# Kernel optimization log

Hardware: AMD Instinct MI355X
Metric: run time of the kernel (lower is better)

## Reference

```python
import jax, jax.numpy as jnp
import numpy as np

# dims: P patches, D=N_azi*N_ele directions, R=P*D radiances, E COO edges,
# T echogram samples, F rfft bins
P, D, R, E, T, NOBJ = 128, 128, 16384, 131072, 1024, 8
F = T // 2 + 1
SR, C_SOUND = 16000.0, 343.0
LOG_GAMMA = float(np.log(1e-3))   # fsm_gamma = 0.001
AIR = 1e-3                        # air absorption coefficient
BOUNCES = 4                       # truncated num_bounces


def setup_inputs():
    key = jax.random.key(0)
    ks = jax.random.split(key, 11)
    return {
        "source_pos": jax.random.normal(ks[0], (3,), jnp.float32) * 2.0,
        "receiver_pos": jax.random.normal(ks[1], (3,), jnp.float32) * 2.0,
        "absorption": jax.random.uniform(ks[2], (NOBJ,), jnp.float32, minval=0.05, maxval=0.6),
        "scattering": jax.random.uniform(ks[3], (NOBJ,), jnp.float32, minval=0.1, maxval=0.9),
        "gk_val": jax.random.uniform(ks[4], (E,), jnp.float32) * 0.1,            # form factors
        "local_kernel_basis": jax.random.uniform(ks[5], (2, D, D), jnp.float32) / D,  # [brdf,Dout,Din]
        "average_distance": jax.random.uniform(ks[6], (R,), jnp.float32) * 10.0 + 1.0,  # meters
        "radiance_pos": jax.random.normal(ks[7], (R, 3), jnp.float32) * 5.0,
        "gk_row": jax.random.randint(ks[8], (E,), 0, R),
        "gk_col": jax.random.randint(ks[9], (E,), 0, R),
        "object_ids": jax.random.randint(ks[10], (P,), 0, NOBJ),
    }


def _path_factor(dist):
    """Frequency-domain factor for a propagation path of length dist [N] -> [N,F].
    Combines fractional delay phase, FSM exponential window gamma^(tau_sec),
    and air absorption exp(-alpha*dist)."""
    freqs = jnp.arange(F, dtype=jnp.float32)
    tau = dist * (SR / C_SOUND)  # delay in samples
    phase = jnp.exp((-2j * np.pi / T) * tau[:, None] * freqs[None, :])
    decay = jnp.exp((LOG_GAMMA / C_SOUND - AIR) * dist)  # fsm + air, per path
    return phase * decay[:, None].astype(phase.dtype)


def reference(source_pos, receiver_pos, absorption, scattering, gk_val,
              local_kernel_basis, average_distance, radiance_pos,
              gk_row, gk_col, object_ids):
    # --- injection: source -> patch-direction radiance [R,F] ---
    d_src = jnp.linalg.norm(radiance_pos - source_pos[None, :], axis=-1)
    g_src = 1.0 / (d_src * d_src + 1e-3)
    rad = g_src[:, None] * _path_factor(d_src)  # complex [R,F]

    # --- BRDF-factorized local kernel: K[p] = sum_b c[b,p] * B[b] ---
    refl = 1.0 - absorption                                   # [NOBJ]
    coeff = jnp.stack([refl * scattering, refl * (1.0 - scattering)])  # [2,NOBJ]
    c_patch = coeff[:, object_ids]                            # [2,P]
    K = jnp.einsum('bp,bde->pde', c_patch, local_kernel_basis)  # [P,Dout,Din]

    prop = _path_factor(average_distance)  # per-radiance transport delay/decay [R,F]

    def bounce(r):
        r = r.reshape(P, D, F)
        r = jnp.einsum('pde,pef->pdf', K.astype(jnp.complex64), r)  # local direction mixing
        r = r.reshape(R, F) * prop
        # sparse COO global kernel: out[row] += val * r[col]
        return jax.ops.segment_sum(gk_val[:, None] * r[gk_col], gk_row, num_segments=R)

    total = rad
    r = rad
    for _ in range(BOUNCES):
        r = bounce(r)
        total = total + r

    # --- detection: patch-direction radiance -> receiver echogram ---
    d_rec = jnp.linalg.norm(radiance_pos - receiver_pos[None, :], axis=-1)
    w_rec = 1.0 / (d_rec * d_rec + 1e-3)
    echo_f = jnp.sum(w_rec[:, None] * _path_factor(d_rec) * total, axis=0)  # [F]

    # FSM correction: divide out the exponential window in time domain
    t = jnp.arange(T, dtype=jnp.float32) / SR
    fsm_window = jnp.exp(LOG_GAMMA * t)
    echogram = jnp.fft.irfft(echo_f, n=T) / fsm_window
    return echogram
```

## Files before the change

### kernel.cpp

```cpp
#include <hip/hip_runtime.h>
#include <math.h>

#define PP 128
#define DD 128
#define RR 16384
#define EE 131072
#define TT 1024
#define FF 513
#define FP 520
#define FPITCH 1056
#define NRB 4096
#define PSTRIDE 528
#define VS16 18

#define TAU_SCALE 46.64723032069971
#define KDECAY   -0.0211392282f
#define LOG_GAMMA -6.907755278982137f
#define TWO_PI    6.283185307179586

typedef __attribute__((ext_vector_type(8))) short bf16x8;
typedef __attribute__((ext_vector_type(4))) float f32x4;
typedef unsigned short u16;

__device__ __forceinline__ u16 f2bf(float x) {
    unsigned u = __float_as_uint(x);
    unsigned r = (u + 0x7fffu + ((u >> 16) & 1u)) >> 16;
    return (u16)r;
}
__device__ __forceinline__ float bf2f(u16 b) {
    return __uint_as_float(((unsigned)b) << 16);
}

__device__ __forceinline__ void pf_sincos(float tau, int f, float* s, float* c) {
    int ti = (int)tau;
    float tf = tau - (float)ti;
    int m = (ti * f) & 1023;
    float u = fmaf(tf, (float)f, (float)m);
    float ang = u * -0.006135923151542565f;
    __sincosf(ang, s, c);
}

__global__ void k_per_row(const float* __restrict__ rpos,
                          const float* __restrict__ spos,
                          const float* __restrict__ cpos,
                          const float* __restrict__ avg_dist,
                          float* __restrict__ per_row) {
    int r = blockIdx.x * blockDim.x + threadIdx.x;
    if (r >= RR) return;
    float x = rpos[3*r], y = rpos[3*r+1], z = rpos[3*r+2];

    float dx = x - spos[0], dy = y - spos[1], dz = z - spos[2];
    float ds = sqrtf(dx*dx + dy*dy + dz*dz);
    per_row[0*RR + r] = (1.0f/(ds*ds + 0.001f)) * expf(KDECAY * ds);
    per_row[1*RR + r] = ds * (float)TAU_SCALE;

    dx = x - cpos[0]; dy = y - cpos[1]; dz = z - cpos[2];
    float dr = sqrtf(dx*dx + dy*dy + dz*dz);
    per_row[2*RR + r] = (1.0f/(dr*dr + 0.001f)) * expf(KDECAY * dr);
    per_row[3*RR + r] = dr * (float)TAU_SCALE;

    float da = avg_dist[r];
    per_row[4*RR + r] = expf(KDECAY * da);
    per_row[5*RR + r] = da * (float)TAU_SCALE;
}

__global__ void k_build_K(const float* __restrict__ absorption,
                          const float* __restrict__ scattering,
                          const int* __restrict__ object_ids,
                          const float* __restrict__ basis,
                          float* __restrict__ Kmat) {
    int idx = blockIdx.x * 256 + threadIdx.x;
    int p  = idx >> 14;
    int de = idx & 16383;
    int obj = object_ids[p];
    float refl = 1.0f - absorption[obj];
    float sc   = scattering[obj];
    Kmat[idx] = refl*sc*basis[de] + refl*(1.0f - sc)*basis[16384 + de];
}

__global__ void k_count(const int* __restrict__ gk_row, int* __restrict__ counts) {
    int e = blockIdx.x * 256 + threadIdx.x;
    atomicAdd(&counts[gk_row[e]], 1);
}

__global__ __launch_bounds__(1024) void k_scan(const int* __restrict__ counts,
                                               int* __restrict__ row_start,
                                               int* __restrict__ cursor) {
    __shared__ int sh[1024];
    int tid = threadIdx.x;
    int base = tid * 16;
    int local[16];
    int sum = 0;
    #pragma unroll
    for (int j = 0; j < 16; j++) { local[j] = sum; sum += counts[base + j]; }
    sh[tid] = sum;
    __syncthreads();
    for (int off = 1; off < 1024; off <<= 1) {
        int v = (tid >= off) ? sh[tid - off] : 0;
        __syncthreads();
        sh[tid] += v;
        __syncthreads();
    }
    int chunk_excl = sh[tid] - sum;
    #pragma unroll
    for (int j = 0; j < 16; j++) {
        int v = chunk_excl + local[j];
        row_start[base + j] = v;
        cursor[base + j] = v;
    }
    if (tid == 1023) row_start[RR] = chunk_excl + sum;
}

__global__ void k_scatter(const int* __restrict__ gk_row,
                          const float* __restrict__ gk_val,
                          const int* __restrict__ gk_col,
                          int* __restrict__ cursor,
                          int2* __restrict__ edge) {
    int e = blockIdx.x * 256 + threadIdx.x;
    int pos = atomicAdd(&cursor[gk_row[e]], 1);
    edge[pos] = make_int2(gk_col[e], __float_as_int(gk_val[e]));
}

__global__ __launch_bounds__(256) void k_init(const float* __restrict__ per_row,
                                              u16* __restrict__ cur,
                                              float* __restrict__ echo) {
    int fl = threadIdx.x & 63, rg = threadIdx.x >> 6;
    int f = blockIdx.x * 64 + fl;
    float ar = 0.f, ai = 0.f;
    int r0 = blockIdx.y * 128;
    if (f < FP) {
        for (int k = rg; k < 128; k += 4) {
            int r = r0 + k;
            float amp = per_row[r], tau = per_row[RR + r];
            float s, c; pf_sincos(tau, f, &s, &c);
            float re = amp * c, im = amp * s;
            unsigned pk = (unsigned)f2bf(re) | ((unsigned)f2bf(im) << 16);
            *(unsigned*)(cur + (size_t)r * FPITCH + f * 2) = pk;
            if (f < FF) {
                float w = per_row[2*RR + r], taur = per_row[3*RR + r];
                float s2, c2; pf_sincos(taur, f, &s2, &c2);
                ar = fmaf(w, c2*re - s2*im, ar);
                ai = fmaf(w, c2*im + s2*re, ai);
            }
        }
    }
    __shared__ float sh[4][64][2];
    sh[rg][fl][0] = ar; sh[rg][fl][1] = ai;
    __syncthreads();
    if (rg == 0 && f < FF) {
        float sx = sh[0][fl][0]+sh[1][fl][0]+sh[2][fl][0]+sh[3][fl][0];
        float sy = sh[0][fl][1]+sh[1][fl][1]+sh[2][fl][1]+sh[3][fl][1];
        atomicAdd(&echo[2*f],   sx);
        atomicAdd(&echo[2*f+1], sy);
    }
}

__global__ __launch_bounds__(256) void k_matmul(const float* __restrict__ Kmat,
                                                const u16* __restrict__ in,
                                                const float* __restrict__ per_row,
                                                u16* __restrict__ out) {
    __shared__ u16 vlds[2][128 * VS16];
    int b = blockIdx.x;
    int xcd = b & 7;
    int g = b >> 3;
    int p = (g >> 3) * 8 + xcd;
    int nq = g & 7;
    int nt0 = nq * 8;
    int ntEnd = (nq == 7) ? 65 : nt0 + 8;

    int tid  = threadIdx.x;
    int wave = tid >> 6;
    int lane = tid & 63;
    int quad = lane >> 4;
    int n    = lane & 15;
    int mt0  = wave << 1;

    bf16x8 Ah[2][4], Al[2][4];
    #pragma unroll
    for (int mi = 0; mi < 2; mi++) {
        const float* kp = Kmat + (p << 14) + ((mt0 + mi) * 16 + n) * 128 + quad * 8;
        #pragma unroll
        for (int kt = 0; kt < 4; kt++) {
            float4 x0 = *(const float4*)(kp + kt * 32);
            float4 x1 = *(const float4*)(kp + kt * 32 + 4);
            float xs[8] = {x0.x,x0.y,x0.z,x0.w,x1.x,x1.y,x1.z,x1.w};
            bf16x8 h, l;
            #pragma unroll
            for (int j = 0; j < 8; j++) {
                u16 hb = f2bf(xs[j]);
                h[j] = (short)hb;
                l[j] = (short)f2bf(xs[j] - bf2f(hb));
            }
            Ah[mi][kt] = h; Al[mi][kt] = l;
        }
    }
    float dec_[2][4];
    float pc[2][4], ps[2][4];
    float rc[2][4], rs[2][4];
    int fq = (n >> 1);
    #pragma unroll
    for (int mi = 0; mi < 2; mi++)
        #pragma unroll
        for (int r = 0; r < 4; r++) {
            int row = (p << 7) + (mt0 + mi) * 16 + quad * 4 + r;
            dec_[mi][r] = per_row[4*RR + row];
            float tau = per_row[5*RR + row];
            pf_sincos(tau, nt0 * 8 + fq, &ps[mi][r], &pc[mi][r]);
            pf_sincos(tau, 8, &rs[mi][r], &rc[mi][r]);
        }

    const u16* pin = in + (size_t)(p << 7) * FPITCH;
    uint4 pk;
    int se = tid >> 1, sc8 = (tid & 1) << 3;
    auto loadTile = [&](int nt) {
        pk = *(const uint4*)(pin + (size_t)se * FPITCH + nt * 16 + sc8);
    };
    auto writeTile = [&](int buf) {
        u16* dst = &vlds[buf][se * VS16 + sc8];
        *(unsigned*)(dst)     = pk.x;
        *(unsigned*)(dst + 2) = pk.y;
        *(unsigned*)(dst + 4) = pk.z;
        *(unsigned*)(dst + 6) = pk.w;
    };

    loadTile(nt0); writeTile(0);
    for (int nt = nt0; nt < ntEnd; nt++) {
        int cb = (nt - nt0) & 1;
        __syncthreads();
        if (nt + 1 < ntEnd) { loadTile(nt + 1); writeTile(cb ^ 1); }

        f32x4 acc0 = {0.f,0.f,0.f,0.f}, acc1 = {0.f,0.f,0.f,0.f};
        const u16* vb = &vlds[cb][0];
        #pragma unroll
        for (int kt = 0; kt < 4; kt++) {
            bf16x8 Bh;
            #pragma unroll
            for (int j = 0; j < 8; j++)
                Bh[j] = (short)vb[(kt*32 + quad*8 + j) * VS16 + n];
            acc0 = __builtin_amdgcn_mfma_f32_16x16x32_bf16(Ah[0][kt], Bh, acc0, 0,0,0);
            acc1 = __builtin_amdgcn_mfma_f32_16x16x32_bf16(Ah[1][kt], Bh, acc1, 0,0,0);
            acc0 = __builtin_amdgcn_mfma_f32_16x16x32_bf16(Al[0][kt], Bh, acc0, 0,0,0);
            acc1 = __builtin_amdgcn_mfma_f32_16x16x32_bf16(Al[1][kt], Bh, acc1, 0,0,0);
        }

        int nfl = nt * 16 + n;
        bool odd = nfl & 1;
        #pragma unroll
        for (int mi = 0; mi < 2; mi++) {
            f32x4 a = mi ? acc1 : acc0;
            #pragma unroll
            for (int r = 0; r < 4; r++) {
                float av = a[r];
                float pv = __shfl_xor(av, 1);
                float s = ps[mi][r], c = pc[mi][r];
                float o = dec_[mi][r] * (odd ? fmaf(av, c,  s*pv)
                                             : fmaf(av, c, -s*pv));
                int row = (p << 7) + (mt0 + mi) * 16 + quad * 4 + r;
                out[(size_t)row * FPITCH + nfl] = f2bf(o);
                float nc = c*rc[mi][r] - s*rs[mi][r];
                float nsv = s*rc[mi][r] + c*rs[mi][r];
                pc[mi][r] = nc; ps[mi][r] = nsv;
            }
        }
    }
}

__global__ __launch_bounds__(512) void k_segsum(const int* __restrict__ row_start,
                                                const int2* __restrict__ edge,
                                                const u16* __restrict__ in,
                                                u16* __restrict__ outp,
                                                const float* __restrict__ per_row,
                                                float2* __restrict__ part,
                                                int store_cur) {
    __shared__ float2 sh[4][128][5];
    int rb = blockIdx.x;
    int fl = threadIdx.x & 127, ry = threadIdx.x >> 7;
    int row = (rb << 2) + ry;
    int s0 = row_start[row], s1 = row_start[row + 1];
    float a0r=0.f,a0i=0.f,a1r=0.f,a1i=0.f,a2r=0.f,a2i=0.f,a3r=0.f,a3i=0.f;
    float t4r=0.f,t4i=0.f;
    bool tail = (fl < 8);
    int t = s0;
    for (; t + 1 < s1; t += 2) {
        int2 e0 = edge[t], e1 = edge[t+1];
        float v0 = __int_as_float(e0.y), v1 = __int_as_float(e1.y);
        const u16* g0p = in + (size_t)e0.x * FPITCH + (fl << 1);
        const u16* g1p = in + (size_t)e1.x * FPITCH + (fl << 1);
        unsigned b00 = *(const unsigned*)(g0p);
        unsigned b01 = *(const unsigned*)(g0p + 256);
        unsigned b02 = *(const unsigned*)(g0p + 512);
        unsigned b03 = *(const unsigned*)(g0p + 768);
        unsigned b10 = *(const unsigned*)(g1p);
        unsigned b11 = *(const unsigned*)(g1p + 256);
        unsigned b12 = *(const unsigned*)(g1p + 512);
        unsigned b13 = *(const unsigned*)(g1p + 768);
        a0r = fmaf(v0, bf2f((u16)(b00 & 0xffffu)), a0r); a0i = fmaf(v0, bf2f((u16)(b00 >> 16)), a0i);
        a1r = fmaf(v0, bf2f((u16)(b01 & 0xffffu)), a1r); a1i = fmaf(v0, bf2f((u16)(b01 >> 16)), a1i);
        a2r = fmaf(v0, bf2f((u16)(b02 & 0xffffu)), a2r); a2i = fmaf(v0, bf2f((u16)(b02 >> 16)), a2i);
        a3r = fmaf(v0, bf2f((u16)(b03 & 0xffffu)), a3r); a3i = fmaf(v0, bf2f((u16)(b03 >> 16)), a3i);
        a0r = fmaf(v1, bf2f((u16)(b10 & 0xffffu)), a0r); a0i = fmaf(v1, bf2f((u16)(b10 >> 16)), a0i);
        a1r = fmaf(v1, bf2f((u16)(b11 & 0xffffu)), a1r); a1i = fmaf(v1, bf2f((u16)(b11 >> 16)), a1i);
        a2r = fmaf(v1, bf2f((u16)(b12 & 0xffffu)), a2r); a2i = fmaf(v1, bf2f((u16)(b12 >> 16)), a2i);
        a3r = fmaf(v1, bf2f((u16)(b13 & 0xffffu)), a3r); a3i = fmaf(v1, bf2f((u16)(b13 >> 16)), a3i);
        if (tail) {
            unsigned b04 = *(const unsigned*)(g0p + 1024);
            unsigned b14 = *(const unsigned*)(g1p + 1024);
            t4r = fmaf(v0, bf2f((u16)(b04 & 0xffffu)), t4r); t4i = fmaf(v0, bf2f((u16)(b04 >> 16)), t4i);
            t4r = fmaf(v1, bf2f((u16)(b14 & 0xffffu)), t4r); t4i = fmaf(v1, bf2f((u16)(b14 >> 16)), t4i);
        }
    }
    if (t < s1) {
        int2 ed = edge[t];
        float v = __int_as_float(ed.y);
        const u16* g = in + (size_t)ed.x * FPITCH + (fl << 1);
        unsigned b0 = *(const unsigned*)(g);
        unsigned b1 = *(const unsigned*)(g + 256);
        unsigned b2 = *(const unsigned*)(g + 512);
        unsigned b3 = *(const unsigned*)(g + 768);
        a0r = fmaf(v, bf2f((u16)(b0 & 0xffffu)), a0r); a0i = fmaf(v, bf2f((u16)(b0 >> 16)), a0i);
        a1r = fmaf(v, bf2f((u16)(b1 & 0xffffu)), a1r); a1i = fmaf(v, bf2f((u16)(b1 >> 16)), a1i);
        a2r = fmaf(v, bf2f((u16)(b2 & 0xffffu)), a2r); a2i = fmaf(v, bf2f((u16)(b2 >> 16)), a2i);
        a3r = fmaf(v, bf2f((u16)(b3 & 0xffffu)), a3r); a3i = fmaf(v, bf2f((u16)(b3 >> 16)), a3i);
        if (tail) {
            unsigned b4 = *(const unsigned*)(g + 1024);
            t4r = fmaf(v, bf2f((u16)(b4 & 0xffffu)), t4r); t4i = fmaf(v, bf2f((u16)(b4 >> 16)), t4i);
        }
    }
    if (store_cur) {
        u16* w = outp + (size_t)row * FPITCH + (fl << 1);
        *(unsigned*)(w)       = (unsigned)f2bf(a0r) | ((unsigned)f2bf(a0i) << 16);
        *(unsigned*)(w + 256) = (unsigned)f2bf(a1r) | ((unsigned)f2bf(a1i) << 16);
        *(unsigned*)(w + 512) = (unsigned)f2bf(a2r) | ((unsigned)f2bf(a2i) << 16);
        *(unsigned*)(w + 768) = (unsigned)f2bf(a3r) | ((unsigned)f2bf(a3i) << 16);
        if (tail)
            *(unsigned*)(w + 1024) = (unsigned)f2bf(t4r) | ((unsigned)f2bf(t4i) << 16);
    }
    float wr = per_row[2*RR + row], taur = per_row[3*RR + row];
    {
        float s, c;
        pf_sincos(taur, fl, &s, &c);
        sh[ry][fl][0] = make_float2(wr*(c*a0r - s*a0i), wr*(c*a0i + s*a0r));
        pf_sincos(taur, fl + 128, &s, &c);
        sh[ry][fl][1] = make_float2(wr*(c*a1r - s*a1i), wr*(c*a1i + s*a1r));
        pf_sincos(taur, fl + 256, &s, &c);
        sh[ry][fl][2] = make_float2(wr*(c*a2r - s*a2i), wr*(c*a2i + s*a2r));
        pf_sincos(taur, fl + 384, &s, &c);
        sh[ry][fl][3] = make_float2(wr*(c*a3r - s*a3i), wr*(c*a3i + s*a3r));
        float2 c4 = make_float2(0.f, 0.f);
        if (tail && (512 + fl) < FF) {
            pf_sincos(taur, 512 + fl, &s, &c);
            c4 = make_float2(wr*(c*t4r - s*t4i), wr*(c*t4i + s*t4r));
        }
        sh[ry][fl][4] = c4;
    }
    __syncthreads();
    if (ry == 0) {
        float2* pp = part + (size_t)rb * PSTRIDE;
        #pragma unroll
        for (int sidx = 0; sidx < 5; sidx++) {
            int fidx = sidx * 128 + fl;
            if (fidx < FP) {
                float2 v0 = sh[0][fl][sidx], v1 = sh[1][fl][sidx];
                float2 v2 = sh[2][fl][sidx], v3 = sh[3][fl][sidx];
                float2 acc = pp[fidx];
                acc.x += v0.x + v1.x + v2.x + v3.x;
                acc.y += v0.y + v1.y + v2.y + v3.y;
                pp[fidx] = acc;
            }
        }
    }
}

__global__ __launch_bounds__(256) void k_fold(const float2* __restrict__ part,
                                              float* __restrict__ echo) {
    int f = blockIdx.x;
    float sx = 0.f, sy = 0.f;
    for (int rb = threadIdx.x; rb < NRB; rb += 256) {
        float2 v = part[(size_t)rb * PSTRIDE + f];
        sx += v.x; sy += v.y;
    }
    for (int off = 32; off >= 1; off >>= 1) {
        sx += __shfl_down(sx, off, 64);
        sy += __shfl_down(sy, off, 64);
    }
    __shared__ float red[2][4];
    int lane = threadIdx.x & 63, w = threadIdx.x >> 6;
    if (lane == 0) { red[0][w] = sx; red[1][w] = sy; }
    __syncthreads();
    if (threadIdx.x == 0) {
        sx = red[0][0]+red[0][1]+red[0][2]+red[0][3];
        sy = red[1][0]+red[1][1]+red[1][2]+red[1][3];
        echo[2*f] += sx;
        echo[2*f+1] += sy;
    }
}

__global__ void k_irfft(const float* __restrict__ echo, float* __restrict__ out) {
    int t = blockIdx.x * blockDim.x + threadIdx.x;
    float acc = echo[0];
    float nyq = echo[2 * 512];
    acc += (t & 1) ? -nyq : nyq;
    for (int f = 1; f < 512; f++) {
        int m = (f * t) & 1023;
        float ang = (float)m * 0.006135923151542565f;
        float s, c; __sincosf(ang, &s, &c);
        acc += 2.0f * (echo[2*f]*c - echo[2*f+1]*s);
    }
    acc *= (1.0f / 1024.0f);
    float tsec = (float)t * (1.0f / 16000.0f);
    float win = expf(LOG_GAMMA * tsec);
    out[t] = acc / win;
}

extern "C" void kernel_launch(void* const* d_in, const int* in_sizes, int n_in,
                              void* d_out, int out_size, void* d_ws, size_t ws_size,
                              hipStream_t stream) {
    const float* source_pos   = (const float*)d_in[0];
    const float* receiver_pos = (const float*)d_in[1];
    const float* absorption   = (const float*)d_in[2];
    const float* scattering   = (const float*)d_in[3];
    const float* gk_val       = (const float*)d_in[4];
    const float* basis        = (const float*)d_in[5];
    const float* avg_dist     = (const float*)d_in[6];
    const float* rpos         = (const float*)d_in[7];
    const int*   gk_row       = (const int*)d_in[8];
    const int*   gk_col       = (const int*)d_in[9];
    const int*   object_ids   = (const int*)d_in[10];
    float* out = (float*)d_out;

    char* base = (char*)d_ws;
    size_t off = 0;
    auto alloc = [&](size_t bytes) -> void* {
        void* ptr = base + off;
        off = (off + bytes + 255) & ~(size_t)255;
        return ptr;
    };
    const size_t PLANE = (size_t)RR * FPITCH + FPITCH;
    float*  Kmat      = (float*)alloc(sizeof(float) * PP * DD * DD);
    u16*    cur       = (u16*)alloc(sizeof(u16) * PLANE);
    u16*    nxt       = (u16*)alloc(sizeof(u16) * PLANE);
    float*  per_row   = (float*)alloc(sizeof(float) * 6 * RR);
    int*    counts    = (int*)alloc(sizeof(int) * RR);
    int*    row_start = (int*)alloc(sizeof(int) * (RR + 1));
    int*    cursor    = (int*)alloc(sizeof(int) * RR);
    int2*   edge      = (int2*)alloc(sizeof(int2) * EE);
    float2* part      = (float2*)alloc(sizeof(float2) * NRB * PSTRIDE);
    float*  echo      = (float*)alloc(sizeof(float) * 1056);

    hipMemsetAsync(counts, 0, sizeof(int) * RR, stream);
    hipMemsetAsync(echo, 0, sizeof(float) * 1056, stream);
    hipMemsetAsync(part, 0, sizeof(float2) * NRB * PSTRIDE, stream);

    k_per_row<<<RR / 256, 256, 0, stream>>>(rpos, source_pos, receiver_pos, avg_dist, per_row);
    k_build_K<<<(PP * DD * DD) / 256, 256, 0, stream>>>(absorption, scattering, object_ids, basis, Kmat);
    k_count<<<EE / 256, 256, 0, stream>>>(gk_row, counts);
    k_scan<<<1, 1024, 0, stream>>>(counts, row_start, cursor);
    k_scatter<<<EE / 256, 256, 0, stream>>>(gk_row, gk_val, gk_col, cursor, edge);
    k_init<<<dim3(9, 128), 256, 0, stream>>>(per_row, cur, echo);

    for (int b = 0; b < 4; b++) {
        k_matmul<<<1024, 256, 0, stream>>>(Kmat, cur, per_row, nxt);
        k_segsum<<<NRB, 512, 0, stream>>>(row_start, edge, nxt, cur,
                                          per_row, part, (b < 3) ? 1 : 0);
    }

    k_fold<<<FF, 256, 0, stream>>>(part, echo);
    k_irfft<<<4, 256, 0, stream>>>(echo, out);
}
```

Measured before the change: 513.5 us.

## Transpose matmul LDS tile, batch segsum rows per block, restructure init with rotation recurrence

The matmul now stores the B tile transposed in LDS, so each lane fetches its bf16x8 operand with one vector load instead of eight strided scalar reads. The segsum kernel handles four rows per thread group (16 rows per block) and accumulates the echo projection in registers, which cuts the partial-sum buffer and its read-modify-write traffic by four. k_init now processes 32 rows per block across all frequencies, using a sincos rotation recurrence instead of a per-frequency sincos call. The trade-offs are scattered 16-bit LDS writes with possible bank conflicts, fewer segsum blocks and therefore less parallelism, and small precision drift from the recurrence.

```diff
diff --git a/kernel.cpp b/kernel.cpp
--- a/kernel.cpp
+++ b/kernel.cpp
@@ -9,9 +9,9 @@
 #define FF 513
 #define FP 520
 #define FPITCH 1056
-#define NRB 4096
+#define NRB 1024
 #define PSTRIDE 528
-#define VS16 18
+#define EPITCH 136
 
 #define TAU_SCALE 46.64723032069971
 #define KDECAY   -0.0211392282f
@@ -124,34 +124,52 @@
 __global__ __launch_bounds__(256) void k_init(const float* __restrict__ per_row,
                                               u16* __restrict__ cur,
                                               float* __restrict__ echo) {
+    __shared__ float2 sh[4][64][9];
     int fl = threadIdx.x & 63, rg = threadIdx.x >> 6;
-    int f = blockIdx.x * 64 + fl;
-    float ar = 0.f, ai = 0.f;
-    int r0 = blockIdx.y * 128;
-    if (f < FP) {
-        for (int k = rg; k < 128; k += 4) {
-            int r = r0 + k;
-            float amp = per_row[r], tau = per_row[RR + r];
-            float s, c; pf_sincos(tau, f, &s, &c);
-            float re = amp * c, im = amp * s;
-            unsigned pk = (unsigned)f2bf(re) | ((unsigned)f2bf(im) << 16);
-            *(unsigned*)(cur + (size_t)r * FPITCH + f * 2) = pk;
+    int r0 = blockIdx.x * 32;
+    float2 eacc[9];
+    #pragma unroll
+    for (int k = 0; k < 9; k++) eacc[k] = make_float2(0.f, 0.f);
+
+    for (int i = 0; i < 8; i++) {
+        int r = r0 + rg + i * 4;
+        float amp = per_row[r],      tau  = per_row[RR + r];
+        float w   = per_row[2*RR+r], taur = per_row[3*RR + r];
+        float s1, c1, rs1, rc1, s2, c2, rs2, rc2;
+        pf_sincos(tau,  fl, &s1, &c1);  pf_sincos(tau,  64, &rs1, &rc1);
+        pf_sincos(taur, fl, &s2, &c2);  pf_sincos(taur, 64, &rs2, &rc2);
+        u16* wrow = cur + (size_t)r * FPITCH;
+        #pragma unroll
+        for (int k = 0; k < 9; k++) {
+            int f = fl + (k << 6);
+            float re = amp * c1, im = amp * s1;
+            if (f < FP)
+                *(unsigned*)(wrow + f * 2) =
+                    (unsigned)f2bf(re) | ((unsigned)f2bf(im) << 16);
             if (f < FF) {
-                float w = per_row[2*RR + r], taur = per_row[3*RR + r];
-                float s2, c2; pf_sincos(taur, f, &s2, &c2);
-                ar = fmaf(w, c2*re - s2*im, ar);
-                ai = fmaf(w, c2*im + s2*re, ai);
-            }
-        }
-    }
-    __shared__ float sh[4][64][2];
-    sh[rg][fl][0] = ar; sh[rg][fl][1] = ai;
+                eacc[k].x = fmaf(w, c2*re - s2*im, eacc[k].x);
+                eacc[k].y = fmaf(w, c2*im + s2*re, eacc[k].y);
+            }
+            float n1c = c1*rc1 - s1*rs1, n1s = s1*rc1 + c1*rs1;
+            c1 = n1c; s1 = n1s;
+            float n2c = c2*rc2 - s2*rs2, n2s = s2*rc2 + c2*rs2;
+            c2 = n2c; s2 = n2s;
+        }
+    }
+    #pragma unroll
+    for (int k = 0; k < 9; k++) sh[rg][fl][k] = eacc[k];
     __syncthreads();
-    if (rg == 0 && f < FF) {
-        float sx = sh[0][fl][0]+sh[1][fl][0]+sh[2][fl][0]+sh[3][fl][0];
-        float sy = sh[0][fl][1]+sh[1][fl][1]+sh[2][fl][1]+sh[3][fl][1];
-        atomicAdd(&echo[2*f],   sx);
-        atomicAdd(&echo[2*f+1], sy);
+    if (rg == 0) {
+        #pragma unroll
+        for (int k = 0; k < 9; k++) {
+            int f = fl + (k << 6);
+            if (f < FF) {
+                float sx = sh[0][fl][k].x + sh[1][fl][k].x + sh[2][fl][k].x + sh[3][fl][k].x;
+                float sy = sh[0][fl][k].y + sh[1][fl][k].y + sh[2][fl][k].y + sh[3][fl][k].y;
+                atomicAdd(&echo[2*f],   sx);
+                atomicAdd(&echo[2*f+1], sy);
+            }
+        }
     }
 }
 
@@ -159,7 +177,7 @@
                                                 const u16* __restrict__ in,
                                                 const float* __restrict__ per_row,
                                                 u16* __restrict__ out) {
-    __shared__ u16 vlds[2][128 * VS16];
+    __shared__ u16 vlds[2][16 * EPITCH];
     int b = blockIdx.x;
     int xcd = b & 7;
     int g = b >> 3;
@@ -216,11 +234,13 @@
         pk = *(const uint4*)(pin + (size_t)se * FPITCH + nt * 16 + sc8);
     };
     auto writeTile = [&](int buf) {
-        u16* dst = &vlds[buf][se * VS16 + sc8];
-        *(unsigned*)(dst)     = pk.x;
-        *(unsigned*)(dst + 2) = pk.y;
-        *(unsigned*)(dst + 4) = pk.z;
-        *(unsigned*)(dst + 6) = pk.w;
+        u16* dst = &vlds[buf][0];
+        unsigned w[4] = {pk.x, pk.y, pk.z, pk.w};
+        #pragma unroll
+        for (int j = 0; j < 8; j++) {
+            u16 v = (u16)(w[j >> 1] >> ((j & 1) * 16));
+            dst[(sc8 + j) * EPITCH + se] = v;
+        }
     };
 
     loadTile(nt0); writeTile(0);
@@ -230,13 +250,10 @@
         if (nt + 1 < ntEnd) { loadTile(nt + 1); writeTile(cb ^ 1); }
 
         f32x4 acc0 = {0.f,0.f,0.f,0.f}, acc1 = {0.f,0.f,0.f,0.f};
-        const u16* vb = &vlds[cb][0];
+        const u16* vb = &vlds[cb][n * EPITCH];
         #pragma unroll
         for (int kt = 0; kt < 4; kt++) {
-            bf16x8 Bh;
-            #pragma unroll
-            for (int j = 0; j < 8; j++)
-                Bh[j] = (short)vb[(kt*32 + quad*8 + j) * VS16 + n];
+            bf16x8 Bh = *(const bf16x8*)(vb + kt * 32 + quad * 8);
             acc0 = __builtin_amdgcn_mfma_f32_16x16x32_bf16(Ah[0][kt], Bh, acc0, 0,0,0);
             acc1 = __builtin_amdgcn_mfma_f32_16x16x32_bf16(Ah[1][kt], Bh, acc1, 0,0,0);
             acc0 = __builtin_amdgcn_mfma_f32_16x16x32_bf16(Al[0][kt], Bh, acc0, 0,0,0);
@@ -275,84 +292,86 @@
     __shared__ float2 sh[4][128][5];
     int rb = blockIdx.x;
     int fl = threadIdx.x & 127, ry = threadIdx.x >> 7;
-    int row = (rb << 2) + ry;
-    int s0 = row_start[row], s1 = row_start[row + 1];
-    float a0r=0.f,a0i=0.f,a1r=0.f,a1i=0.f,a2r=0.f,a2i=0.f,a3r=0.f,a3i=0.f;
-    float t4r=0.f,t4i=0.f;
     bool tail = (fl < 8);
-    int t = s0;
-    for (; t + 1 < s1; t += 2) {
-        int2 e0 = edge[t], e1 = edge[t+1];
-        float v0 = __int_as_float(e0.y), v1 = __int_as_float(e1.y);
-        const u16* g0p = in + (size_t)e0.x * FPITCH + (fl << 1);
-        const u16* g1p = in + (size_t)e1.x * FPITCH + (fl << 1);
-        unsigned b00 = *(const unsigned*)(g0p);
-        unsigned b01 = *(const unsigned*)(g0p + 256);
-        unsigned b02 = *(const unsigned*)(g0p + 512);
-        unsigned b03 = *(const unsigned*)(g0p + 768);
-        unsigned b10 = *(const unsigned*)(g1p);
-        unsigned b11 = *(const unsigned*)(g1p + 256);
-        unsigned b12 = *(const unsigned*)(g1p + 512);
-        unsigned b13 = *(const unsigned*)(g1p + 768);
-        a0r = fmaf(v0, bf2f((u16)(b00 & 0xffffu)), a0r); a0i = fmaf(v0, bf2f((u16)(b00 >> 16)), a0i);
-        a1r = fmaf(v0, bf2f((u16)(b01 & 0xffffu)), a1r); a1i = fmaf(v0, bf2f((u16)(b01 >> 16)), a1i);
-        a2r = fmaf(v0, bf2f((u16)(b02 & 0xffffu)), a2r); a2i = fmaf(v0, bf2f((u16)(b02 >> 16)), a2i);
-        a3r = fmaf(v0, bf2f((u16)(b03 & 0xffffu)), a3r); a3i = fmaf(v0, bf2f((u16)(b03 >> 16)), a3i);
-        a0r = fmaf(v1, bf2f((u16)(b10 & 0xffffu)), a0r); a0i = fmaf(v1, bf2f((u16)(b10 >> 16)), a0i);
-        a1r = fmaf(v1, bf2f((u16)(b11 & 0xffffu)), a1r); a1i = fmaf(v1, bf2f((u16)(b11 >> 16)), a1i);
-        a2r = fmaf(v1, bf2f((u16)(b12 & 0xffffu)), a2r); a2i = fmaf(v1, bf2f((u16)(b12 >> 16)), a2i);
-        a3r = fmaf(v1, bf2f((u16)(b13 & 0xffffu)), a3r); a3i = fmaf(v1, bf2f((u16)(b13 >> 16)), a3i);
-        if (tail) {
-            unsigned b04 = *(const unsigned*)(g0p + 1024);
-            unsigned b14 = *(const unsigned*)(g1p + 1024);
-            t4r = fmaf(v0, bf2f((u16)(b04 & 0xffffu)), t4r); t4i = fmaf(v0, bf2f((u16)(b04 >> 16)), t4i);
-            t4r = fmaf(v1, bf2f((u16)(b14 & 0xffffu)), t4r); t4i = fmaf(v1, bf2f((u16)(b14 >> 16)), t4i);
-        }
-    }
-    if (t < s1) {
-        int2 ed = edge[t];
-        float v = __int_as_float(ed.y);
-        const u16* g = in + (size_t)ed.x * FPITCH + (fl << 1);
-        unsigned b0 = *(const unsigned*)(g);
-        unsigned b1 = *(const unsigned*)(g + 256);
-        unsigned b2 = *(const unsigned*)(g + 512);
-        unsigned b3 = *(const unsigned*)(g + 768);
-        a0r = fmaf(v, bf2f((u16)(b0 & 0xffffu)), a0r); a0i = fmaf(v, bf2f((u16)(b0 >> 16)), a0i);
-        a1r = fmaf(v, bf2f((u16)(b1 & 0xffffu)), a1r); a1i = fmaf(v, bf2f((u16)(b1 >> 16)), a1i);
-        a2r = fmaf(v, bf2f((u16)(b2 & 0xffffu)), a2r); a2i = fmaf(v, bf2f((u16)(b2 >> 16)), a2i);
-        a3r = fmaf(v, bf2f((u16)(b3 & 0xffffu)), a3r); a3i = fmaf(v, bf2f((u16)(b3 >> 16)), a3i);
-        if (tail) {
-            unsigned b4 = *(const unsigned*)(g + 1024);
-            t4r = fmaf(v, bf2f((u16)(b4 & 0xffffu)), t4r); t4i = fmaf(v, bf2f((u16)(b4 >> 16)), t4i);
-        }
-    }
-    if (store_cur) {
-        u16* w = outp + (size_t)row * FPITCH + (fl << 1);
-        *(unsigned*)(w)       = (unsigned)f2bf(a0r) | ((unsigned)f2bf(a0i) << 16);
-        *(unsigned*)(w + 256) = (unsigned)f2bf(a1r) | ((unsigned)f2bf(a1i) << 16);
-        *(unsigned*)(w + 512) = (unsigned)f2bf(a2r) | ((unsigned)f2bf(a2i) << 16);
-        *(unsigned*)(w + 768) = (unsigned)f2bf(a3r) | ((unsigned)f2bf(a3i) << 16);
-        if (tail)
-            *(unsigned*)(w + 1024) = (unsigned)f2bf(t4r) | ((unsigned)f2bf(t4i) << 16);
-    }
-    float wr = per_row[2*RR + row], taur = per_row[3*RR + row];
-    {
+    float2 e0 = {0.f,0.f}, e1 = {0.f,0.f}, e2 = {0.f,0.f}, e3 = {0.f,0.f}, e4 = {0.f,0.f};
+
+    for (int i = 0; i < 4; i++) {
+        int row = (rb << 4) + (ry << 2) + i;
+        int s0 = row_start[row], s1 = row_start[row + 1];
+        float a0r=0.f,a0i=0.f,a1r=0.f,a1i=0.f,a2r=0.f,a2i=0.f,a3r=0.f,a3i=0.f;
+        float t4r=0.f,t4i=0.f;
+        int t = s0;
+        for (; t + 1 < s1; t += 2) {
+            int2 ed0 = edge[t], ed1 = edge[t+1];
+            float v0 = __int_as_float(ed0.y), v1 = __int_as_float(ed1.y);
+            const u16* g0p = in + (size_t)ed0.x * FPITCH + (fl << 1);
+            const u16* g1p = in + (size_t)ed1.x * FPITCH + (fl << 1);
+            unsigned b00 = *(const unsigned*)(g0p);
+            unsigned b01 = *(const unsigned*)(g0p + 256);
+            unsigned b02 = *(const unsigned*)(g0p + 512);
+            unsigned b03 = *(const unsigned*)(g0p + 768);
+            unsigned b10 = *(const unsigned*)(g1p);
+            unsigned b11 = *(const unsigned*)(g1p + 256);
+            unsigned b12 = *(const unsigned*)(g1p + 512);
+            unsigned b13 = *(const unsigned*)(g1p + 768);
+            a0r = fmaf(v0, bf2f((u16)(b00 & 0xffffu)), a0r); a0i = fmaf(v0, bf2f((u16)(b00 >> 16)), a0i);
+            a1r = fmaf(v0, bf2f((u16)(b01 & 0xffffu)), a1r); a1i = fmaf(v0, bf2f((u16)(b01 >> 16)), a1i);
+            a2r = fmaf(v0, bf2f((u16)(b02 & 0xffffu)), a2r); a2i = fmaf(v0, bf2f((u16)(b02 >> 16)), a2i);
+            a3r = fmaf(v0, bf2f((u16)(b03 & 0xffffu)), a3r); a3i = fmaf(v0, bf2f((u16)(b03 >> 16)), a3i);
+            a0r = fmaf(v1, bf2f((u16)(b10 & 0xffffu)), a0r); a0i = fmaf(v1, bf2f((u16)(b10 >> 16)), a0i);
+            a1r = fmaf(v1, bf2f((u16)(b11 & 0xffffu)), a1r); a1i = fmaf(v1, bf2f((u16)(b11 >> 16)), a1i);
+            a2r = fmaf(v1, bf2f((u16)(b12 & 0xffffu)), a2r); a2i = fmaf(v1, bf2f((u16)(b12 >> 16)), a2i);
+            a3r = fmaf(v1, bf2f((u16)(b13 & 0xffffu)), a3r); a3i = fmaf(v1, bf2f((u16)(b13 >> 16)), a3i);
+            if (tail) {
+                unsigned b04 = *(const unsigned*)(g0p + 1024);
+                unsigned b14 = *(const unsigned*)(g1p + 1024);
+                t4r = fmaf(v0, bf2f((u16)(b04 & 0xffffu)), t4r); t4i = fmaf(v0, bf2f((u16)(b04 >> 16)), t4i);
+                t4r = fmaf(v1, bf2f((u16)(b14 & 0xffffu)), t4r); t4i = fmaf(v1, bf2f((u16)(b14 >> 16)), t4i);
+            }
+        }
+        if (t < s1) {
+            int2 ed = edge[t];
+            float v = __int_as_float(ed.y);
+            const u16* g = in + (size_t)ed.x * FPITCH + (fl << 1);
+            unsigned b0 = *(const unsigned*)(g);
+            unsigned b1 = *(const unsigned*)(g + 256);
+            unsigned b2 = *(const unsigned*)(g + 512);
+            unsigned b3 = *(const unsigned*)(g + 768);
+            a0r = fmaf(v, bf2f((u16)(b0 & 0xffffu)), a0r); a0i = fmaf(v, bf2f((u16)(b0 >> 16)), a0i);
+            a1r = fmaf(v, bf2f((u16)(b1 & 0xffffu)), a1r); a1i = fmaf(v, bf2f((u16)(b1 >> 16)), a1i);
+            a2r = fmaf(v, bf2f((u16)(b2 & 0xffffu)), a2r); a2i = fmaf(v, bf2f((u16)(b2 >> 16)), a2i);
+            a3r = fmaf(v, bf2f((u16)(b3 & 0xffffu)), a3r); a3i = fmaf(v, bf2f((u16)(b3 >> 16)), a3i);
+            if (tail) {
+                unsigned b4 = *(const unsigned*)(g + 1024);
+                t4r = fmaf(v, bf2f((u16)(b4 & 0xffffu)), t4r); t4i = fmaf(v, bf2f((u16)(b4 >> 16)), t4i);
+            }
+        }
+        if (store_cur) {
+            u16* w = outp + (size_t)row * FPITCH + (fl << 1);
+            *(unsigned*)(w)       = (unsigned)f2bf(a0r) | ((unsigned)f2bf(a0i) << 16);
+            *(unsigned*)(w + 256) = (unsigned)f2bf(a1r) | ((unsigned)f2bf(a1i) << 16);
+            *(unsigned*)(w + 512) = (unsigned)f2bf(a2r) | ((unsigned)f2bf(a2i) << 16);
+            *(unsigned*)(w + 768) = (unsigned)f2bf(a3r) | ((unsigned)f2bf(a3i) << 16);
+            if (tail)
+                *(unsigned*)(w + 1024) = (unsigned)f2bf(t4r) | ((unsigned)f2bf(t4i) << 16);
+        }
+        float wr = per_row[2*RR + row], taur = per_row[3*RR + row];
         float s, c;
         pf_sincos(taur, fl, &s, &c);
-        sh[ry][fl][0] = make_float2(wr*(c*a0r - s*a0i), wr*(c*a0i + s*a0r));
+        e0.x = fmaf(wr, c*a0r - s*a0i, e0.x); e0.y = fmaf(wr, c*a0i + s*a0r, e0.y);
         pf_sincos(taur, fl + 128, &s, &c);
-        sh[ry][fl][1] = make_float2(wr*(c*a1r - s*a1i), wr*(c*a1i + s*a1r));
+        e1.x = fmaf(wr, c*a1r - s*a1i, e1.x); e1.y = fmaf(wr, c*a1i + s*a1r, e1.y);
         pf_sincos(taur, fl + 256, &s, &c);
-        sh[ry][fl][2] = make_float2(wr*(c*a2r - s*a2i), wr*(c*a2i + s*a2r));
+        e2.x = fmaf(wr, c*a2r - s*a2i, e2.x); e2.y = fmaf(wr, c*a2i + s*a2r, e2.y);
         pf_sincos(taur, fl + 384, &s, &c);
-        sh[ry][fl][3] = make_float2(wr*(c*a3r - s*a3i), wr*(c*a3i + s*a3r));
-        float2 c4 = make_float2(0.f, 0.f);
+        e3.x = fmaf(wr, c*a3r - s*a3i, e3.x); e3.y = fmaf(wr, c*a3i + s*a3r, e3.y);
         if (tail && (512 + fl) < FF) {
             pf_sincos(taur, 512 + fl, &s, &c);
-            c4 = make_float2(wr*(c*t4r - s*t4i), wr*(c*t4i + s*t4r));
-        }
-        sh[ry][fl][4] = c4;
-    }
+            e4.x = fmaf(wr, c*t4r - s*t4i, e4.x); e4.y = fmaf(wr, c*t4i + s*t4r, e4.y);
+        }
+    }
+    sh[ry][fl][0] = e0; sh[ry][fl][1] = e1; sh[ry][fl][2] = e2;
+    sh[ry][fl][3] = e3; sh[ry][fl][4] = e4;
     __syncthreads();
     if (ry == 0) {
         float2* pp = part + (size_t)rb * PSTRIDE;
@@ -456,7 +475,7 @@
     k_count<<<EE / 256, 256, 0, stream>>>(gk_row, counts);
     k_scan<<<1, 1024, 0, stream>>>(counts, row_start, cursor);
     k_scatter<<<EE / 256, 256, 0, stream>>>(gk_row, gk_val, gk_col, cursor, edge);
-    k_init<<<dim3(9, 128), 256, 0, stream>>>(per_row, cur, echo);
+    k_init<<<512, 256, 0, stream>>>(per_row, cur, echo);
 
     for (int b = 0; b < 4; b++) {
         k_matmul<<<1024, 256, 0, stream>>>(Kmat, cur, per_row, nxt);
```

Measured after the change: 485.3 us. 1.06x faster.
